# Kernel optimization log

Measured on AMD Instinct MI355X. Metric: run time of the kernel, lower is better.

Reference implementation:

```python
import jax, jax.numpy as jnp
import numpy as np

B, C, H, W = 8, 512, 32, 32


def setup_inputs() -> dict:
    key = jax.random.key(0)
    ks = jax.random.split(key, 7)
    s = 0.02  # typical conv init scale
    return {
        "x": jax.random.normal(ks[0], (B, C, H, W), dtype=jnp.float32),
        "Wq": jax.random.normal(ks[1], (C, C), dtype=jnp.float32) * s,
        "bq": jax.random.normal(ks[2], (C,), dtype=jnp.float32) * s,
        "Wk": jax.random.normal(ks[3], (C, C), dtype=jnp.float32) * s,
        "bk": jax.random.normal(ks[4], (C,), dtype=jnp.float32) * s,
        "W6": jax.random.normal(ks[5], (C, C), dtype=jnp.float32) * s,
        "b6": jax.random.normal(ks[6], (C,), dtype=jnp.float32) * s,
    }


def _gam(x, Wq, bq, Wk, bk, W6, b6):
    b, c, h, w = x.shape
    hw = h * w
    scale = 1.0 / (c ** 0.5)
    # 1x1 convs == per-pixel channel matmuls (torch conv weight [out,in,1,1])
    q = jnp.einsum('bchw,dc->bhwd', x, Wq) + bq          # [B,H,W,C]
    q = q.reshape(b * hw, c)                              # query rows
    k = jnp.einsum('bchw,dc->bdhw', x, Wk) + bk[None, :, None, None]
    k = jnp.transpose(k, (1, 0, 2, 3)).reshape(c, b * hw)  # [C, B*HW]
    xw = (q.astype(jnp.float32) @ k.astype(jnp.float32))   # [B*HW, B*HW]
    xw = xw.reshape(b * hw, b, hw)
    xw = jnp.max(xw, axis=-1)                              # max over keys' spatial dim
    xw = jnp.mean(xw, axis=-1)                             # mean over key images
    xw = xw.reshape(b, hw) * scale
    xw = jax.nn.softmax(xw, axis=-1).astype(x.dtype)
    xw = xw.reshape(b, 1, h, w)
    x5 = x * xw
    return jnp.einsum('bchw,dc->bdhw', x5, W6) + b6[None, :, None, None]


def reference(x, Wq, bq, Wk, bk, W6, b6):
    x_new = _gam(x, Wq, bq, Wk, bk, W6, b6)
    # prototype: mean over batch and spatial dims, keep channels
    x_proto = jnp.mean(x_new.astype(jnp.float32), axis=(0, 2, 3)).astype(x.dtype)
    return x * x_proto[None, :, None, None]
```

## Files before the change

### kernel.cpp

```cpp
#include <hip/hip_runtime.h>
#include <hip/hip_bf16.h>

typedef __bf16 bf16_t;
typedef __bf16 bf16x8 __attribute__((ext_vector_type(8)));
typedef float f32x4 __attribute__((ext_vector_type(4)));

#define B_   8
#define C_   512
#define HW_  1024
#define NPIX 8192

typedef __attribute__((address_space(3))) void lds_vp;
typedef const __attribute__((address_space(1))) void gbl_vp;
__device__ __forceinline__ void gload_lds16(const void* g, void* l) {
    __builtin_amdgcn_global_load_lds((gbl_vp*)g, (lds_vp*)l, 16, 0, 0);
}

__device__ __forceinline__ void stage128x64(const bf16_t* __restrict__ g, int ldk,
                                            bf16_t* lds, int tid) {
    int w64 = tid & ~63;
#pragma unroll
    for (int s = 0; s < 4; ++s) {
        int u = s * 256 + tid;
        const bf16_t* src = g + (size_t)(u >> 3) * ldk + (u & 7) * 8;
        gload_lds16((const void*)src, (void*)(lds + (size_t)(s * 256 + w64) * 8));
    }
}

__global__ void k_cvt_w(const float* __restrict__ Wq, const float* __restrict__ Wk,
                        bf16_t* __restrict__ wq, bf16_t* __restrict__ wk) {
    int i = blockIdx.x * 256 + threadIdx.x;
    wq[i] = (bf16_t)Wq[i];
    wk[i] = (bf16_t)Wk[i];
}

__global__ void k_transpose(const float* __restrict__ x, bf16_t* __restrict__ xT) {
    __shared__ bf16_t tile[64 * 66];
    int p0 = blockIdx.x * 64, c0 = blockIdx.y * 64, b = blockIdx.z;
    int t = threadIdx.x;
#pragma unroll
    for (int s = 0; s < 16; ++s) {
        int u = s * 256 + t;
        int cr = u >> 6, pc = u & 63;
        tile[cr * 66 + pc] = (bf16_t)x[((size_t)(b * C_ + c0 + cr)) * HW_ + p0 + pc];
    }
    __syncthreads();
#pragma unroll
    for (int s = 0; s < 16; ++s) {
        int u = s * 256 + t;
        int pr = u >> 6, cc = u & 63;
        xT[((size_t)(b * HW_ + p0 + pr)) * C_ + c0 + cc] = tile[cc * 66 + pr];
    }
}

__launch_bounds__(256, 2)
__global__ void k_gemm_qk(const bf16_t* __restrict__ xT,
                          const bf16_t* __restrict__ wq, const bf16_t* __restrict__ wk,
                          const float* __restrict__ bq, const float* __restrict__ bk,
                          bf16_t* __restrict__ qo, bf16_t* __restrict__ ko) {
    __shared__ bf16_t As[128 * 64];
    __shared__ bf16_t Bs[128 * 64];
    int bid = blockIdx.x;
    int mtile = bid >> 3;
    int nt = bid & 7;
    const bf16_t* wsel = (nt < 4) ? wq : wk;
    const float*  bsel = (nt < 4) ? bq : bk;
    bf16_t*       osel = (nt < 4) ? qo : ko;
    int nb = (nt & 3) * 128;
    int i0 = mtile * 128;
    int tid = threadIdx.x;
    int lane = tid & 63, w = tid >> 6;
    int wr = w >> 1, wc = w & 1, lr = lane & 15, lg = lane >> 4;

    f32x4 acc[4][4];
#pragma unroll
    for (int mi = 0; mi < 4; ++mi)
#pragma unroll
        for (int ni = 0; ni < 4; ++ni)
#pragma unroll
            for (int r = 0; r < 4; ++r) acc[mi][ni][r] = 0.f;

    for (int kt = 0; kt < 8; ++kt) {
        int k0 = kt * 64;
        stage128x64(xT + (size_t)i0 * 512 + k0, 512, As, tid);
        stage128x64(wsel + (size_t)nb * 512 + k0, 512, Bs, tid);
        __syncthreads();
#pragma unroll
        for (int kk = 0; kk < 2; ++kk) {
            bf16x8 af[4], bfr[4];
#pragma unroll
            for (int mi = 0; mi < 4; ++mi)
                af[mi] = *reinterpret_cast<const bf16x8*>(
                    &As[(wr * 64 + mi * 16 + lr) * 64 + kk * 32 + lg * 8]);
#pragma unroll
            for (int ni = 0; ni < 4; ++ni)
                bfr[ni] = *reinterpret_cast<const bf16x8*>(
                    &Bs[(wc * 64 + ni * 16 + lr) * 64 + kk * 32 + lg * 8]);
#pragma unroll
            for (int mi = 0; mi < 4; ++mi)
#pragma unroll
                for (int ni = 0; ni < 4; ++ni)
                    acc[mi][ni] = __builtin_amdgcn_mfma_f32_16x16x32_bf16(
                        af[mi], bfr[ni], acc[mi][ni], 0, 0, 0);
        }
        __syncthreads();
    }
#pragma unroll
    for (int ni = 0; ni < 4; ++ni) {
        int col = nb + wc * 64 + ni * 16 + lr;
        float bias = bsel[col];
#pragma unroll
        for (int mi = 0; mi < 4; ++mi) {
            int rowb = i0 + wr * 64 + mi * 16 + lg * 4;
#pragma unroll
            for (int r = 0; r < 4; ++r)
                osel[(size_t)(rowb + r) * 512 + col] = (bf16_t)(acc[mi][ni][r] + bias);
        }
    }
}


#define STAGE_AR(REG, OFF)                                                         \
    gload_lds16((const void*)(q + srcA0 + (OFF)),                                  \
                (void*)(lds + (REG) * 8192 + ld0));                                \
    gload_lds16((const void*)(q + srcA1 + (OFF)),                                  \
                (void*)(lds + (REG) * 8192 + ld1));

#define STAGE_BR(REG, OFF)                                                         \
    gload_lds16((const void*)(kb + srcB0 + (OFF)),                                 \
                (void*)(lds + 32768 + (REG) * 8192 + ld0));                        \
    gload_lds16((const void*)(kb + srcB1 + (OFF)),                                 \
                (void*)(lds + 32768 + (REG) * 8192 + ld1));

#define PHASE(REGI, MH, STAGE_STMT, VM_STMT)                                       \
    {                                                                              \
        const bf16_t* Ab = lds + (REGI) * 8192;                                    \
        const bf16_t* Bb = lds + 32768 + (REGI) * 8192;                            \
        _Pragma("unroll")                                                          \
        for (int mi = 0; mi < 4; ++mi)                                             \
            af[mi] = *(const bf16x8*)(Ab + aoff + ((MH) * 4 + mi) * 512);          \
        if ((MH) == 0) {                                                           \
            _Pragma("unroll")                                                      \
            for (int ni = 0; ni < 4; ++ni)                                         \
                bf[ni] = *(const bf16x8*)(Bb + boff + ni * 512);                   \
        }                                                                          \
        STAGE_STMT;                                                                \
        __builtin_amdgcn_s_barrier();                                              \
        asm volatile("s_waitcnt lgkmcnt(0)" ::: "memory");                         \
        __builtin_amdgcn_sched_barrier(0);                                         \
        __builtin_amdgcn_s_setprio(1);                                             \
        _Pragma("unroll")                                                          \
        for (int mi = 0; mi < 4; ++mi)                                             \
            _Pragma("unroll")                                                      \
            for (int ni = 0; ni < 4; ++ni)                                         \
                acc[(MH) * 4 + mi][ni] = __builtin_amdgcn_mfma_f32_16x16x32_bf16(  \
                    af[mi], bf[ni], acc[(MH) * 4 + mi][ni], 0, 0, 0);              \
        __builtin_amdgcn_s_setprio(0);                                             \
        VM_STMT;                                                                   \
        __builtin_amdgcn_s_barrier();                                              \
    }

__global__ __launch_bounds__(512, 2)
void k_gemm_max8(const bf16_t* __restrict__ q, const bf16_t* __restrict__ kp,
                 float* __restrict__ Mout) {
    __shared__ __align__(16) bf16_t lds[65536];
    int bid = blockIdx.x;
    int img = bid & 7;
    int qp = bid >> 3;
    int i0 = qp * 256;
    const bf16_t* kb = kp + (size_t)img * HW_ * C_;
    int tid = threadIdx.x;
    int lane = tid & 63, w = tid >> 6;
    int wr = w >> 2, wc = w & 3;
    int lr = lane & 15, lg = lane >> 4;
    int rowh = lr >> 1;
    int sA = (lg * 2 + (lr & 1)) ^ (rowh & 7);
    int aoff = (wr * 64 + rowh) * 64 + sA * 8;
    int boff = (wc * 32 + rowh) * 64 + sA * 8;

    int s0 = (tid & 7) ^ ((tid >> 3) & 7);
    int r0 = (tid >> 3) * 2 + (s0 & 1);
    size_t srcA0 = (size_t)(i0 + r0) * 512 + (s0 >> 1) * 8;
    size_t srcA1 = srcA0 + (size_t)128 * 512;
    size_t srcB0 = (size_t)r0 * 512 + (s0 >> 1) * 8;
    size_t srcB1 = srcB0 + (size_t)128 * 512;
    int ld0 = (tid & ~63) * 8, ld1 = (512 + (tid & ~63)) * 8;

    f32x4 acc[8][4];
    bf16x8 af[4], bf[4];
    float rm[8][4];
#pragma unroll
    for (int mi = 0; mi < 8; ++mi)
#pragma unroll
        for (int ni = 0; ni < 4; ++ni)
#pragma unroll
            for (int r = 0; r < 4; ++r) acc[mi][ni][r] = 0.f;
#pragma unroll
    for (int mi = 0; mi < 8; ++mi)
#pragma unroll
        for (int r = 0; r < 4; ++r) rm[mi][r] = -3.4e38f;

    STAGE_BR(0, 0) STAGE_AR(0, 0) STAGE_BR(1, 32) STAGE_AR(1, 32)
    STAGE_BR(2, 64) STAGE_AR(2, 64) STAGE_BR(3, 96)
    asm volatile("s_waitcnt vmcnt(6)" ::: "memory");
    __builtin_amdgcn_s_barrier();

    for (int i = 0; i < 16; ++i) {
        int t1 = 2 * i + 1, t2 = t1 + 1, t3 = t1 + 2;
        int a1 = (t1 & 7) * 64, a2 = (t2 & 7) * 64, a3 = (t3 & 7) * 64;
        int b2 = ((t2 >> 3) << 17) + a2, b3 = ((t3 >> 3) << 17) + a3;
        bool s = (i < 15);
        PHASE(0, 0, { STAGE_AR(3, a1 + 32) }, {})
        PHASE(0, 1, { if (s) { STAGE_BR(0, b2) } }, {})
        PHASE(1, 0, { if (s) { STAGE_AR(0, a2) } }, {})
        PHASE(1, 1, { if (s) { STAGE_BR(1, b2 + 32) } },
              { if (s) { asm volatile("s_waitcnt vmcnt(6)" ::: "memory"); }
                else   { asm volatile("s_waitcnt vmcnt(0)" ::: "memory"); } })
        PHASE(2, 0, { if (s) { STAGE_AR(1, a2 + 32) } }, {})
        PHASE(2, 1, { if (s) { STAGE_BR(2, b3) } }, {})
        PHASE(3, 0, { if (s) { STAGE_AR(2, a3) } }, {})
        PHASE(3, 1, { if (s) { STAGE_BR(3, b3 + 32) } },
              { if (s) { asm volatile("s_waitcnt vmcnt(6)" ::: "memory"); } })
        if ((i & 3) == 3) {
#pragma unroll
            for (int mi = 0; mi < 8; ++mi)
#pragma unroll
                for (int r = 0; r < 4; ++r) {
                    float v = fmaxf(fmaxf(acc[mi][0][r], acc[mi][1][r]),
                                    fmaxf(acc[mi][2][r], acc[mi][3][r]));
                    rm[mi][r] = fmaxf(rm[mi][r], v);
#pragma unroll
                    for (int ni = 0; ni < 4; ++ni) acc[mi][ni][r] = 0.f;
                }
        }
    }

#pragma unroll
    for (int mi = 0; mi < 8; ++mi)
#pragma unroll
        for (int r = 0; r < 4; ++r) {
            float v = rm[mi][r];
#pragma unroll
            for (int off = 1; off < 16; off <<= 1) v = fmaxf(v, __shfl_xor(v, off));
            rm[mi][r] = v;
        }
    float* sm = (float*)lds;
    if (lr == 0) {
#pragma unroll
        for (int mi = 0; mi < 8; ++mi)
#pragma unroll
            for (int r = 0; r < 4; ++r)
                sm[wc * 256 + wr * 128 + mi * 16 + lg * 4 + r] = rm[mi][r];
    }
    __syncthreads();
    if (tid < 256) {
        float v = fmaxf(fmaxf(sm[tid], sm[256 + tid]),
                        fmaxf(sm[512 + tid], sm[768 + tid]));
        Mout[(size_t)(i0 + tid) * 8 + img] = v;
    }
}

__global__ void k_softmax(const float* __restrict__ Mout, float* __restrict__ wsm) {
    int b = blockIdx.x;
    int t = threadIdx.x;
    __shared__ float red[16];
    const float scale = 0.044194173824159216f;
    float s[4];
#pragma unroll
    for (int i = 0; i < 4; ++i) {
        int p = t + i * 256;
        const float* row = &Mout[(size_t)(b * 1024 + p) * 8];
        float acc = 0.f;
#pragma unroll
        for (int j = 0; j < 8; ++j) acc += row[j];
        s[i] = acc * (scale / 8.0f);
    }
    float m = fmaxf(fmaxf(s[0], s[1]), fmaxf(s[2], s[3]));
#pragma unroll
    for (int off = 1; off < 64; off <<= 1) m = fmaxf(m, __shfl_xor(m, off));
    if ((t & 63) == 0) red[t >> 6] = m;
    __syncthreads();
    float m4 = fmaxf(fmaxf(red[0], red[1]), fmaxf(red[2], red[3]));
    float e[4], sum = 0.f;
#pragma unroll
    for (int i = 0; i < 4; ++i) { e[i] = __expf(s[i] - m4); sum += e[i]; }
#pragma unroll
    for (int off = 1; off < 64; off <<= 1) sum += __shfl_xor(sum, off);
    if ((t & 63) == 0) red[8 + (t >> 6)] = sum;
    __syncthreads();
    float tot = red[8] + red[9] + red[10] + red[11];
    float inv = 1.0f / tot;
#pragma unroll
    for (int i = 0; i < 4; ++i) wsm[b * 1024 + t + i * 256] = e[i] * inv;
}

__global__ void k_reduce_y(const float* __restrict__ x, const float* __restrict__ wsm,
                           float* __restrict__ y) {
    int c = blockIdx.x;
    int t = threadIdx.x;
    float acc = 0.f;
    for (int b = 0; b < 8; ++b) {
        const float* xb = x + ((size_t)(b * C_ + c)) * HW_;
        const float* wb = wsm + b * HW_;
#pragma unroll
        for (int i = 0; i < 4; ++i) {
            int p = t + i * 256;
            acc += xb[p] * wb[p];
        }
    }
#pragma unroll
    for (int off = 1; off < 64; off <<= 1) acc += __shfl_xor(acc, off);
    __shared__ float red[4];
    if ((t & 63) == 0) red[t >> 6] = acc;
    __syncthreads();
    if (t == 0) y[c] = (red[0] + red[1] + red[2] + red[3]) * (1.0f / 8192.0f);
}

__global__ void k_proto(const float* __restrict__ W6, const float* __restrict__ b6,
                        const float* __restrict__ y, float* __restrict__ proto) {
    int d = blockIdx.x;
    int lane = threadIdx.x;
    float acc = 0.f;
#pragma unroll
    for (int i = 0; i < 8; ++i)
        acc += W6[(size_t)d * C_ + lane + i * 64] * y[lane + i * 64];
#pragma unroll
    for (int off = 1; off < 64; off <<= 1) acc += __shfl_xor(acc, off);
    if (lane == 0) proto[d] = acc + b6[d];
}

__global__ void k_final(const float* __restrict__ x, const float* __restrict__ proto,
                        float* __restrict__ out) {
    int idx = blockIdx.x * 256 + threadIdx.x;
    float4 v = ((const float4*)x)[idx];
    int c = (idx >> 8) & 511;
    float p = proto[c];
    v.x *= p; v.y *= p; v.z *= p; v.w *= p;
    ((float4*)out)[idx] = v;
}

extern "C" void kernel_launch(void* const* d_in, const int* in_sizes, int n_in,
                              void* d_out, int out_size, void* d_ws, size_t ws_size,
                              hipStream_t stream) {
    const float* x  = (const float*)d_in[0];
    const float* Wq = (const float*)d_in[1];
    const float* bq = (const float*)d_in[2];
    const float* Wk = (const float*)d_in[3];
    const float* bk = (const float*)d_in[4];
    const float* W6 = (const float*)d_in[5];
    const float* b6 = (const float*)d_in[6];
    float* out = (float*)d_out;

    char* ws = (char*)d_ws;
    bf16_t* xT    = (bf16_t*)(ws);
    float*  Mout  = (float*)(ws);
    bf16_t* wqb   = (bf16_t*)(ws + 8388608);
    bf16_t* wkb   = (bf16_t*)(ws + 8912896);
    bf16_t* qb    = (bf16_t*)(ws + 9437184);
    bf16_t* kb    = (bf16_t*)(ws + 17825792);
    float*  wsm   = (float*)(ws + 26476544);
    float*  yv    = (float*)(ws + 26509312);
    float*  proto = (float*)(ws + 26511360);

    hipLaunchKernelGGL(k_cvt_w, dim3(1024), dim3(256), 0, stream, Wq, Wk, wqb, wkb);
    hipLaunchKernelGGL(k_transpose, dim3(16, 8, 8), dim3(256), 0, stream, x, xT);
    hipLaunchKernelGGL(k_gemm_qk, dim3(512), dim3(256), 0, stream,
                       xT, wqb, wkb, bq, bk, qb, kb);
    hipLaunchKernelGGL(k_gemm_max8, dim3(256), dim3(512), 0, stream, qb, kb, Mout);
    hipLaunchKernelGGL(k_softmax, dim3(8), dim3(256), 0, stream, Mout, wsm);
    hipLaunchKernelGGL(k_reduce_y, dim3(512), dim3(256), 0, stream, x, wsm, yv);
    hipLaunchKernelGGL(k_proto, dim3(512), dim3(64), 0, stream, W6, b6, yv, proto);
    hipLaunchKernelGGL(k_final, dim3(4096), dim3(256), 0, stream, x, proto, out);
}
```

Baseline: 110.3 us.

## Restage GEMM-max LDS tiles as 64-wide K double buffers with new swizzle

```diff
diff --git a/kernel.cpp b/kernel.cpp
--- a/kernel.cpp
+++ b/kernel.cpp
@@ -120,29 +120,36 @@
 }
 
 
-#define STAGE_AR(REG, OFF)                                                         \
-    gload_lds16((const void*)(q + srcA0 + (OFF)),                                  \
-                (void*)(lds + (REG) * 8192 + ld0));                                \
-    gload_lds16((const void*)(q + srcA1 + (OFF)),                                  \
-                (void*)(lds + (REG) * 8192 + ld1));
-
-#define STAGE_BR(REG, OFF)                                                         \
-    gload_lds16((const void*)(kb + srcB0 + (OFF)),                                 \
-                (void*)(lds + 32768 + (REG) * 8192 + ld0));                        \
-    gload_lds16((const void*)(kb + srcB1 + (OFF)),                                 \
-                (void*)(lds + 32768 + (REG) * 8192 + ld1));
-
-#define PHASE(REGI, MH, STAGE_STMT, VM_STMT)                                       \
+#define STAGE_A(RH, D, T)                                                          \
+    gload_lds16((const void*)(q + srcA + (size_t)((RH) * 128) * 512 +              \
+                              ((T) & 7) * 64),                                     \
+                (void*)(ldsb + (RH) * 32768 + (D) * 16384 + ldw));                 \
+    gload_lds16((const void*)(q + srcA + (size_t)((RH) * 128 + 64) * 512 +         \
+                              ((T) & 7) * 64),                                     \
+                (void*)(ldsb + (RH) * 32768 + (D) * 16384 + 8192 + ldw));
+
+#define STAGE_B(RH, D, T)                                                          \
+    gload_lds16((const void*)(kb + srcB +                                          \
+                              (size_t)(((T) >> 3) * 256 + (RH) * 128) * 512 +      \
+                              ((T) & 7) * 64),                                     \
+                (void*)(ldsb + 65536 + (RH) * 32768 + (D) * 16384 + ldw));         \
+    gload_lds16((const void*)(kb + srcB +                                          \
+                              (size_t)(((T) >> 3) * 256 + (RH) * 128 + 64) * 512 + \
+                              ((T) & 7) * 64),                                     \
+                (void*)(ldsb + 65536 + (RH) * 32768 + (D) * 16384 + 8192 + ldw));
+
+#define PHASE(D, KH, MH, STAGE_STMT, VM_STMT)                                      \
     {                                                                              \
-        const bf16_t* Ab = lds + (REGI) * 8192;                                    \
-        const bf16_t* Bb = lds + 32768 + (REGI) * 8192;                            \
+        const char* Ab = ldsb + wr * 32768 + (D) * 16384 + (KH) * 64;              \
+        const char* Bb = ldsb + 65536 + (wc >> 1) * 32768 + (D) * 16384 +          \
+                         (KH) * 64;                                                \
         _Pragma("unroll")                                                          \
         for (int mi = 0; mi < 4; ++mi)                                             \
-            af[mi] = *(const bf16x8*)(Ab + aoff + ((MH) * 4 + mi) * 512);          \
+            af[mi] = *(const bf16x8*)(Ab + aswz + ((MH) * 4 + mi) * 2048);         \
         if ((MH) == 0) {                                                           \
             _Pragma("unroll")                                                      \
             for (int ni = 0; ni < 4; ++ni)                                         \
-                bf[ni] = *(const bf16x8*)(Bb + boff + ni * 512);                   \
+                bf[ni] = *(const bf16x8*)(Bb + bswz + ni * 2048);                  \
         }                                                                          \
         STAGE_STMT;                                                                \
         __builtin_amdgcn_s_barrier();                                              \
@@ -164,6 +171,7 @@
 void k_gemm_max8(const bf16_t* __restrict__ q, const bf16_t* __restrict__ kp,
                  float* __restrict__ Mout) {
     __shared__ __align__(16) bf16_t lds[65536];
+    char* ldsb = (char*)lds;
     int bid = blockIdx.x;
     int img = bid & 7;
     int qp = bid >> 3;
@@ -173,18 +181,15 @@
     int lane = tid & 63, w = tid >> 6;
     int wr = w >> 2, wc = w & 3;
     int lr = lane & 15, lg = lane >> 4;
-    int rowh = lr >> 1;
-    int sA = (lg * 2 + (lr & 1)) ^ (rowh & 7);
-    int aoff = (wr * 64 + rowh) * 64 + sA * 8;
-    int boff = (wc * 32 + rowh) * 64 + sA * 8;
-
-    int s0 = (tid & 7) ^ ((tid >> 3) & 7);
-    int r0 = (tid >> 3) * 2 + (s0 & 1);
-    size_t srcA0 = (size_t)(i0 + r0) * 512 + (s0 >> 1) * 8;
-    size_t srcA1 = srcA0 + (size_t)128 * 512;
-    size_t srcB0 = (size_t)r0 * 512 + (s0 >> 1) * 8;
-    size_t srcB1 = srcB0 + (size_t)128 * 512;
-    int ld0 = (tid & ~63) * 8, ld1 = (512 + (tid & ~63)) * 8;
+    int kswz = (lg * 16) ^ ((lr & 4) << 3);
+    int aswz = lr * 128 + kswz;
+    int bswz = ((wc & 1) * 64 + lr) * 128 + kswz;
+
+    int srow = ((tid >> 6) << 3) + ((tid >> 3) & 7);
+    int sk = ((tid & 7) << 3) ^ ((tid & 32) >> 1);
+    size_t srcA = (size_t)(i0 + srow) * 512 + sk;
+    size_t srcB = (size_t)srow * 512 + sk;
+    int ldw = (tid >> 6) * 1024;
 
     f32x4 acc[8][4];
     bf16x8 af[4], bf[4];
@@ -200,27 +205,25 @@
 #pragma unroll
         for (int r = 0; r < 4; ++r) rm[mi][r] = -3.4e38f;
 
-    STAGE_BR(0, 0) STAGE_AR(0, 0) STAGE_BR(1, 32) STAGE_AR(1, 32)
-    STAGE_BR(2, 64) STAGE_AR(2, 64) STAGE_BR(3, 96)
-    asm volatile("s_waitcnt vmcnt(6)" ::: "memory");
+    STAGE_B(0, 0, 0) STAGE_A(0, 0, 0) STAGE_B(1, 0, 0) STAGE_A(1, 0, 0)
+    STAGE_B(0, 1, 1)
+    asm volatile("s_waitcnt vmcnt(2)" ::: "memory");
     __builtin_amdgcn_s_barrier();
 
     for (int i = 0; i < 16; ++i) {
-        int t1 = 2 * i + 1, t2 = t1 + 1, t3 = t1 + 2;
-        int a1 = (t1 & 7) * 64, a2 = (t2 & 7) * 64, a3 = (t3 & 7) * 64;
-        int b2 = ((t2 >> 3) << 17) + a2, b3 = ((t3 >> 3) << 17) + a3;
+        int tb = 2 * i + 1, tc = 2 * i + 2, td = 2 * i + 3;
         bool s = (i < 15);
-        PHASE(0, 0, { STAGE_AR(3, a1 + 32) }, {})
-        PHASE(0, 1, { if (s) { STAGE_BR(0, b2) } }, {})
-        PHASE(1, 0, { if (s) { STAGE_AR(0, a2) } }, {})
-        PHASE(1, 1, { if (s) { STAGE_BR(1, b2 + 32) } },
-              { if (s) { asm volatile("s_waitcnt vmcnt(6)" ::: "memory"); }
+        PHASE(0, 0, 0, { STAGE_A(0, 1, tb) }, {})
+        PHASE(0, 0, 1, { STAGE_B(1, 1, tb) }, {})
+        PHASE(0, 1, 0, { STAGE_A(1, 1, tb) }, {})
+        PHASE(0, 1, 1, { if (s) { STAGE_B(0, 0, tc) } },
+              { if (s) { asm volatile("s_waitcnt vmcnt(2)" ::: "memory"); }
                 else   { asm volatile("s_waitcnt vmcnt(0)" ::: "memory"); } })
-        PHASE(2, 0, { if (s) { STAGE_AR(1, a2 + 32) } }, {})
-        PHASE(2, 1, { if (s) { STAGE_BR(2, b3) } }, {})
-        PHASE(3, 0, { if (s) { STAGE_AR(2, a3) } }, {})
-        PHASE(3, 1, { if (s) { STAGE_BR(3, b3 + 32) } },
-              { if (s) { asm volatile("s_waitcnt vmcnt(6)" ::: "memory"); } })
+        PHASE(1, 0, 0, { if (s) { STAGE_A(0, 0, tc) } }, {})
+        PHASE(1, 0, 1, { if (s) { STAGE_B(1, 0, tc) } }, {})
+        PHASE(1, 1, 0, { if (s) { STAGE_A(1, 0, tc) } }, {})
+        PHASE(1, 1, 1, { if (s) { STAGE_B(0, 1, td) } },
+              { if (s) { asm volatile("s_waitcnt vmcnt(2)" ::: "memory"); } })
         if ((i & 3) == 3) {
 #pragma unroll
             for (int mi = 0; mi < 8; ++mi)
```

New measurement: 107.3 us. 1.03x faster.
